# Optimization experiments

Measured on AMD Instinct MI355X. Metric: run time of the kernel, lower is better.

Reference implementation:

```python
import jax, jax.numpy as jnp
import numpy as np

EMBED = 768
HIDDEN = 768
HEADS = 12
HEAD_DIM = HIDDEN // HEADS


def setup_inputs() -> dict:
    key = jax.random.key(0)
    ks = jax.random.split(key, 9)
    B, S = 16, 512
    lim = 1.0 / np.sqrt(EMBED)
    def lin(kw, kb):
        W = jax.random.uniform(kw, (EMBED, HIDDEN), jnp.float32, -lim, lim)
        b = jax.random.uniform(kb, (HIDDEN,), jnp.float32, -lim, lim)
        return W, b
    Wq, bq = lin(ks[0], ks[1])
    Wk, bk = lin(ks[2], ks[3])
    Wv, bv = lin(ks[4], ks[5])
    inp = jax.random.normal(ks[6], (B, S, EMBED), jnp.float32)
    mask = jax.random.randint(ks[7], (B, S), 0, 2).astype(jnp.float32)
    return {"input": inp, "input_mask": mask,
            "Wq": Wq, "bq": bq, "Wk": Wk, "bk": bk, "Wv": Wv, "bv": bv}


def reference(input, input_mask, Wq, bq, Wk, bk, Wv, bv):
    B, S, _ = input.shape
    # projections -> (B, H, S, D)
    def proj(W, b):
        x = jnp.einsum('bse,eh->bsh', input, W) + b
        return x.reshape(B, S, HEADS, HEAD_DIM).transpose(0, 2, 1, 3)
    Q = proj(Wq, bq)
    K = proj(Wk, bk)
    V = proj(Wv, bv)
    # scores (B, H, S, S), additive mask over keys
    scores = jnp.einsum('bhqd,bhkd->bhqk', Q, K) / jnp.sqrt(jnp.float32(HEAD_DIM))
    bias = (input_mask * -1e9)[:, None, None, :]  # (B,1,1,S) broadcast over heads & queries
    weight = jax.nn.softmax(scores + bias, axis=-1)
    out = jnp.einsum('bhqk,bhkd->bhqd', weight, V)
    return out.transpose(0, 2, 1, 3).reshape(B, S, HIDDEN)
```

## Files before the change

### kernel.cpp

```cpp
#include <hip/hip_runtime.h>
#include <hip/hip_bf16.h>
#include <cstdint>
#include <cstddef>

#define B_  16
#define S_  512
#define E_  768
#define NH_ 12
#define D_  64
#define M_  (B_*S_)

typedef unsigned short u16;
typedef __attribute__((ext_vector_type(4))) float f32x4;
typedef __attribute__((ext_vector_type(8))) short bf16x8;

#define LOG2E 1.4426950408889634f

__device__ __forceinline__ u16 f2bf(float f){
  union { float fv; uint32_t u; } v; v.fv = f;
  uint32_t u = v.u;
  uint32_t r = u + 0x7fffu + ((u >> 16) & 1u);
  return (u16)(r >> 16);
}

__device__ __forceinline__ void gload_lds16(const u16* g, u16* l){
  __builtin_amdgcn_global_load_lds(
      (const __attribute__((address_space(1))) void*)g,
      (__attribute__((address_space(3))) void*)l, 16, 0, 0);
}

__device__ __forceinline__ uint4 pack8(const float4& a, const float4& b){
  float2 p01; p01.x = a.x; p01.y = a.y;
  float2 p23; p23.x = a.z; p23.y = a.w;
  float2 p45; p45.x = b.x; p45.y = b.y;
  float2 p67; p67.x = b.z; p67.y = b.w;
  __hip_bfloat162 h0 = __float22bfloat162_rn(p01);
  __hip_bfloat162 h1 = __float22bfloat162_rn(p23);
  __hip_bfloat162 h2 = __float22bfloat162_rn(p45);
  __hip_bfloat162 h3 = __float22bfloat162_rn(p67);
  uint4 r;
  r.x = *reinterpret_cast<const unsigned int*>(&h0);
  r.y = *reinterpret_cast<const unsigned int*>(&h1);
  r.z = *reinterpret_cast<const unsigned int*>(&h2);
  r.w = *reinterpret_cast<const unsigned int*>(&h3);
  return r;
}

__global__ __launch_bounds__(256) void prep_kernel(
    const float* __restrict__ Wq, const float* __restrict__ Wk,
    const float* __restrict__ Wv, u16* __restrict__ WtBase)
{
  __shared__ float t[32][33];
  const int tt = blockIdx.x;
  int z = tt / 576, rem = tt % 576;
  int byi = rem / 24, bxi = rem % 24;
  const float* W = (z == 0) ? Wq : ((z == 1) ? Wk : Wv);
  u16* Wt = WtBase + (size_t)z * E_ * E_;
  int bx0 = bxi * 32, by0 = byi * 32;
  int tx = threadIdx.x & 31, ty = threadIdx.x >> 5;
  #pragma unroll
  for (int i = 0; i < 32; i += 8)
    t[ty + i][tx] = W[(size_t)(by0 + ty + i) * E_ + bx0 + tx];
  __syncthreads();
  #pragma unroll
  for (int i = 0; i < 32; i += 8)
    Wt[(size_t)(bx0 + ty + i) * E_ + by0 + tx] = f2bf(t[tx][ty + i]);
}

__global__ __launch_bounds__(512) void qkv_gemm_kernel(
    const float* __restrict__ X, const u16* __restrict__ WtBase,
    const float* __restrict__ bq, const float* __restrict__ bk, const float* __restrict__ bv,
    u16* __restrict__ Qb, u16* __restrict__ Kb, u16* __restrict__ VtB)
{
  extern __shared__ u16 lds[];
  u16* ldsA = lds;
  u16* ldsB = lds + 2 * 8192;

  const int z = blockIdx.z;
  const u16* Wt = WtBase + (size_t)z * E_ * E_;
  const float* bias = (z == 0) ? bq : ((z == 1) ? bk : bv);
  const int m0 = blockIdx.x * 128;
  const int n0 = blockIdx.y * 256;
  const int tid = threadIdx.x;
  const int lane = tid & 63;
  const int wave = tid >> 6;
  const int wm = wave & 1, wn = wave >> 1;
  const int col0 = lane & 15, quad = lane >> 4;
  const int rslot = quad*16 + (col0 ^ (quad << 1));
  const int oct_l = lane >> 4;
  const int row_l = (lane & 15) ^ (oct_l << 1);

  f32x4 acc[4][4];
  #pragma unroll
  for (int i = 0; i < 4; ++i)
    #pragma unroll
    for (int j = 0; j < 4; ++j)
      acc[i][j] = (f32x4){0.f, 0.f, 0.f, 0.f};

  const float* pX  = X  + (size_t)(m0 + wave*16 + row_l) * E_ + oct_l*8;
  const u16*   pB0 = Wt + (size_t)(n0 + wave*32 + row_l) * E_ + oct_l*8;
  const u16*   pB1 = pB0 + (size_t)16 * E_;

  float4 ax[4];
  auto loadA = [&](int k0){
    const float* p0 = pX + k0;
    const float* p1 = pX + k0 + 32;
    ax[0] = *reinterpret_cast<const float4*>(p0);
    ax[1] = *reinterpret_cast<const float4*>(p0 + 4);
    ax[2] = *reinterpret_cast<const float4*>(p1);
    ax[3] = *reinterpret_cast<const float4*>(p1 + 4);
  };
  auto writeA = [&](int buf){
    u16* la = ldsA + buf * 8192;
    uint4 w0 = pack8(ax[0], ax[1]);
    uint4 w1 = pack8(ax[2], ax[3]);
    *reinterpret_cast<uint4*>(&la[(2*wave    )*512 + lane*8]) = w0;
    *reinterpret_cast<uint4*>(&la[(2*wave + 1)*512 + lane*8]) = w1;
  };
  auto stageB = [&](int k0, int buf){
    u16* lb = ldsB + buf * 16384;
    gload_lds16(pB0 + k0,      lb + (4*wave    )*512);
    gload_lds16(pB0 + k0 + 32, lb + (4*wave + 1)*512);
    gload_lds16(pB1 + k0,      lb + (4*wave + 2)*512);
    gload_lds16(pB1 + k0 + 32, lb + (4*wave + 3)*512);
  };

  auto compute = [&](int buf){
    const u16* la = ldsA + buf * 8192;
    const u16* lb = ldsB + buf * 16384;
    #pragma unroll
    for (int ks = 0; ks < 2; ++ks){
      bf16x8 af[4], bfr[4];
      #pragma unroll
      for (int mi = 0; mi < 4; ++mi)
        af[mi] = *reinterpret_cast<const bf16x8*>(&la[((wm*4 + mi)*2 + ks)*512 + rslot*8]);
      #pragma unroll
      for (int ni = 0; ni < 4; ++ni)
        bfr[ni] = *reinterpret_cast<const bf16x8*>(&lb[((wn*4 + ni)*2 + ks)*512 + rslot*8]);
      #pragma unroll
      for (int mi = 0; mi < 4; ++mi)
        #pragma unroll
        for (int ni = 0; ni < 4; ++ni)
          acc[mi][ni] = __builtin_amdgcn_mfma_f32_16x16x32_bf16(af[mi], bfr[ni], acc[mi][ni], 0, 0, 0);
    }
  };

  stageB(0, 0);
  loadA(0);
  writeA(0);

  #pragma unroll 1
  for (int st = 0; st < 12; ++st){
    const int cur = st & 1;
    __syncthreads();
    if (st < 11){
      stageB((st + 1) * 64, cur ^ 1);
      loadA((st + 1) * 64);
    }
    compute(cur);
    if (st < 11) writeA(cur ^ 1);
  }

  #pragma unroll
  for (int mi = 0; mi < 4; ++mi){
    #pragma unroll
    for (int ni = 0; ni < 4; ++ni){
      int n = n0 + wn*64 + ni*16 + col0;
      float bval = bias[n];
      int h = n >> 6, d = n & 63;
      #pragma unroll
      for (int r = 0; r < 4; ++r){
        int m = m0 + wm*64 + mi*16 + quad*4 + r;
        int b = m >> 9, s = m & 511;
        u16 obf = f2bf(acc[mi][ni][r] + bval);
        size_t bh = (size_t)b * NH_ + h;
        if (z == 0)      Qb[(bh * S_ + s) * D_ + d] = obf;
        else if (z == 1) Kb[(bh * S_ + s) * D_ + d] = obf;
        else             VtB[(bh * D_ + d) * S_ + s] = obf;
      }
    }
  }
}

__global__ __launch_bounds__(256) void attn_kernel(
    const u16* __restrict__ Qb, const u16* __restrict__ Kb, const u16* __restrict__ VtB,
    const float* __restrict__ mask, float* __restrict__ out)
{
  __shared__ u16 lK[2][8 * 512];
  __shared__ u16 lV[2][8 * 512];
  __shared__ u16 lP[8 * 1024];
  __shared__ float biasS[S_];
  const int bh = blockIdx.x;
  const int qt = blockIdx.y;
  const int b = bh / NH_, h = bh % NH_;
  const int tid = threadIdx.x, lane = tid & 63, wave = tid >> 6;
  const int col0 = lane & 15, quad = lane >> 4;
  const int ls = lane & 15, lk = lane >> 4;
  const float C1 = 0.125f * LOG2E;

  for (int i = tid; i < S_; i += 256)
    biasS[i] = mask[b * S_ + i] * (-1.0e9f * LOG2E);

  const u16* Kbh = Kb  + (size_t)bh * S_ * D_;
  const u16* Vbh = VtB + (size_t)bh * D_ * S_;

  bf16x8 qf[2][2];
  #pragma unroll
  for (int g = 0; g < 2; ++g){
    int qrow = qt*128 + wave*32 + g*16 + col0;
    #pragma unroll
    for (int ks = 0; ks < 2; ++ks)
      qf[g][ks] = *reinterpret_cast<const bf16x8*>(
          Qb + ((size_t)bh * S_ + qrow) * D_ + ks*32 + quad*8);
  }

  uint4 rg[4];
  auto issue = [&](int st){
    if (wave < 2){
      #pragma unroll
      for (int gg = 0; gg < 4; ++gg){
        int c = wave*4 + gg, ks = c >> 2, nt = c & 3;
        rg[gg] = *reinterpret_cast<const uint4*>(
            Kbh + (size_t)(st*64 + nt*16 + ls) * D_ + ks*32 + lk*8);
      }
    } else {
      #pragma unroll
      for (int gg = 0; gg < 4; ++gg){
        int c = (wave - 2)*4 + gg, ks2 = c >> 2, nd = c & 3;
        rg[gg] = *reinterpret_cast<const uint4*>(
            Vbh + (size_t)(nd*16 + ls) * S_ + st*64 + ks2*32 + lk*8);
      }
    }
  };
  issue(0);

  f32x4 o[2][4];
  #pragma unroll
  for (int g = 0; g < 2; ++g)
    #pragma unroll
    for (int i = 0; i < 4; ++i) o[g][i] = (f32x4){0.f, 0.f, 0.f, 0.f};
  float psum[2] = {0.f, 0.f};

  #pragma unroll 1
  for (int st = 0; st < 8; ++st){
    const int cur = st & 1;
    if (wave < 2){
      #pragma unroll
      for (int gg = 0; gg < 4; ++gg)
        *reinterpret_cast<uint4*>(&lK[cur][(wave*4 + gg)*512 + lane*8]) = rg[gg];
    } else {
      #pragma unroll
      for (int gg = 0; gg < 4; ++gg)
        *reinterpret_cast<uint4*>(&lV[cur][((wave - 2)*4 + gg)*512 + lane*8]) = rg[gg];
    }
    __syncthreads();
    if (st < 7) issue(st + 1);

    f32x4 sc[2][4];
    #pragma unroll
    for (int g = 0; g < 2; ++g)
      #pragma unroll
      for (int nt = 0; nt < 4; ++nt) sc[g][nt] = (f32x4){0.f, 0.f, 0.f, 0.f};
    #pragma unroll
    for (int ks = 0; ks < 2; ++ks){
      bf16x8 kf[4];
      #pragma unroll
      for (int nt = 0; nt < 4; ++nt)
        kf[nt] = *reinterpret_cast<const bf16x8*>(&lK[cur][(ks*4 + nt)*512 + lane*8]);
      #pragma unroll
      for (int g = 0; g < 2; ++g)
        #pragma unroll
        for (int nt = 0; nt < 4; ++nt)
          sc[g][nt] = __builtin_amdgcn_mfma_f32_16x16x32_bf16(kf[nt], qf[g][ks], sc[g][nt], 0, 0, 0);
    }

    float4 bb[4];
    #pragma unroll
    for (int nt = 0; nt < 4; ++nt)
      bb[nt] = *reinterpret_cast<const float4*>(&biasS[st*64 + nt*16 + quad*4]);

    #pragma unroll
    for (int g = 0; g < 2; ++g){
      #pragma unroll
      for (int nt = 0; nt < 4; ++nt){
        float p0 = exp2f(sc[g][nt][0] * C1 + bb[nt].x);
        float p1 = exp2f(sc[g][nt][1] * C1 + bb[nt].y);
        float p2 = exp2f(sc[g][nt][2] * C1 + bb[nt].z);
        float p3 = exp2f(sc[g][nt][3] * C1 + bb[nt].w);
        psum[g] += (p0 + p1) + (p2 + p3);
        float2 ab; ab.x = p0; ab.y = p1;
        float2 cd; cd.x = p2; cd.y = p3;
        __hip_bfloat162 h01 = __float22bfloat162_rn(ab);
        __hip_bfloat162 h23 = __float22bfloat162_rn(cd);
        uint2 pw;
        pw.x = *reinterpret_cast<unsigned int*>(&h01);
        pw.y = *reinterpret_cast<unsigned int*>(&h23);
        int addr = (wave*2 + g)*1024 + (nt >> 1)*512
                 + (((nt & 1)*2 + (quad >> 1))*16 + col0)*8 + (quad & 1)*4;
        *reinterpret_cast<uint2*>(&lP[addr]) = pw;
      }
    }

    #pragma unroll
    for (int ks2 = 0; ks2 < 2; ++ks2){
      bf16x8 pf0 = *reinterpret_cast<const bf16x8*>(&lP[(wave*2 + 0)*1024 + ks2*512 + lane*8]);
      bf16x8 pf1 = *reinterpret_cast<const bf16x8*>(&lP[(wave*2 + 1)*1024 + ks2*512 + lane*8]);
      #pragma unroll
      for (int nd = 0; nd < 4; ++nd){
        bf16x8 vf = *reinterpret_cast<const bf16x8*>(&lV[cur][(ks2*4 + nd)*512 + lane*8]);
        o[0][nd] = __builtin_amdgcn_mfma_f32_16x16x32_bf16(pf0, vf, o[0][nd], 0, 0, 0);
        o[1][nd] = __builtin_amdgcn_mfma_f32_16x16x32_bf16(pf1, vf, o[1][nd], 0, 0, 0);
      }
    }
  }

  #pragma unroll
  for (int g = 0; g < 2; ++g){
    float tot = psum[g];
    tot += __shfl_xor(tot, 16, 64);
    tot += __shfl_xor(tot, 32, 64);
    #pragma unroll
    for (int r = 0; r < 4; ++r){
      int s = qt*128 + wave*32 + g*16 + quad*4 + r;
      float lr = __shfl(tot, (lane & 48) | (quad*4 + r), 64);
      float inv = 1.0f / lr;
      #pragma unroll
      for (int nd = 0; nd < 4; ++nd){
        int d = nd*16 + col0;
        out[((size_t)b * S_ + s) * E_ + h*D_ + d] = o[g][nd][r] * inv;
      }
    }
  }
}

extern "C" void kernel_launch(void* const* d_in, const int* in_sizes, int n_in,
                              void* d_out, int out_size, void* d_ws, size_t ws_size,
                              hipStream_t stream){
  const float* X    = (const float*)d_in[0];
  const float* mask = (const float*)d_in[1];
  const float* Wq   = (const float*)d_in[2];
  const float* bq   = (const float*)d_in[3];
  const float* Wk   = (const float*)d_in[4];
  const float* bk   = (const float*)d_in[5];
  const float* Wv   = (const float*)d_in[6];
  const float* bv   = (const float*)d_in[7];
  float* out = (float*)d_out;

  u16* Wt = (u16*)d_ws;
  u16* Qb = Wt + (size_t)3 * E_ * E_;
  u16* Kb = Qb + (size_t)M_ * E_;
  u16* Vt = Kb + (size_t)M_ * E_;

  prep_kernel<<<1728, 256, 0, stream>>>(Wq, Wk, Wv, Wt);
  qkv_gemm_kernel<<<dim3(64, 3, 3), 512, 98304, stream>>>(X, Wt, bq, bk, bv, Qb, Kb, Vt);
  attn_kernel<<<dim3(192, 4), 256, 0, stream>>>(Qb, Kb, Vt, mask, out);
}
```

Baseline: 228.3 us.

## Fuse QKV projection and attention into one per-(batch,head) kernel

Replaces the separate QKV GEMM and attention kernels with one kernel per (batch, head). Each block computes Q, K and V for all 512 tokens of its head directly into LDS, then runs attention from LDS, so Q/K/V never go through global memory. Block indices are mapped so that related blocks share an XCD. The costs are that only 192 blocks of 512 threads run, each with about 146KB of LDS (low occupancy). X is also read directly from global without LDS staging, and each block rereads its batch's X rows once for each of Q, K and V.

```diff
diff --git a/kernel.cpp b/kernel.cpp
--- a/kernel.cpp
+++ b/kernel.cpp
@@ -67,226 +67,170 @@
     Wt[(size_t)(bx0 + ty + i) * E_ + by0 + tx] = f2bf(t[tx][ty + i]);
 }
 
-__global__ __launch_bounds__(512) void qkv_gemm_kernel(
+__global__ __launch_bounds__(512) void fused_kernel(
     const float* __restrict__ X, const u16* __restrict__ WtBase,
     const float* __restrict__ bq, const float* __restrict__ bk, const float* __restrict__ bv,
-    u16* __restrict__ Qb, u16* __restrict__ Kb, u16* __restrict__ VtB)
+    const float* __restrict__ mask, float* __restrict__ out)
 {
   extern __shared__ u16 lds[];
-  u16* ldsA = lds;
-  u16* ldsB = lds + 2 * 8192;
-
-  const int z = blockIdx.z;
-  const u16* Wt = WtBase + (size_t)z * E_ * E_;
-  const float* bias = (z == 0) ? bq : ((z == 1) ? bk : bv);
-  const int m0 = blockIdx.x * 128;
-  const int n0 = blockIdx.y * 256;
-  const int tid = threadIdx.x;
-  const int lane = tid & 63;
-  const int wave = tid >> 6;
-  const int wm = wave & 1, wn = wave >> 1;
+  u16* lK  = lds;
+  u16* lV  = lds + 32768;
+  u16* lBP = lds + 65536;
+  float* biasS = (float*)(lds + 73728);
+
+  const int blk = blockIdx.x;
+  const int xcd = blk & 7, idx = blk >> 3;
+  const int b = xcd * 2 + (idx >= 12 ? 1 : 0);
+  const int h = (idx >= 12) ? (idx - 12) : idx;
+
+  const int tid = threadIdx.x, lane = tid & 63, wave = tid >> 6;
   const int col0 = lane & 15, quad = lane >> 4;
   const int rslot = quad*16 + (col0 ^ (quad << 1));
   const int oct_l = lane >> 4;
   const int row_l = (lane & 15) ^ (oct_l << 1);
+  const float C1 = 0.125f * LOG2E;
+
+  if (tid < S_) biasS[tid] = mask[b * S_ + tid] * (-1.0e9f * LOG2E);
+
+  const float* Xrow = X + ((size_t)(b * S_ + wave * 64)) * E_;
 
   f32x4 acc[4][4];
   #pragma unroll
   for (int i = 0; i < 4; ++i)
     #pragma unroll
-    for (int j = 0; j < 4; ++j)
-      acc[i][j] = (f32x4){0.f, 0.f, 0.f, 0.f};
-
-  const float* pX  = X  + (size_t)(m0 + wave*16 + row_l) * E_ + oct_l*8;
-  const u16*   pB0 = Wt + (size_t)(n0 + wave*32 + row_l) * E_ + oct_l*8;
-  const u16*   pB1 = pB0 + (size_t)16 * E_;
-
-  float4 ax[4];
-  auto loadA = [&](int k0){
-    const float* p0 = pX + k0;
-    const float* p1 = pX + k0 + 32;
-    ax[0] = *reinterpret_cast<const float4*>(p0);
-    ax[1] = *reinterpret_cast<const float4*>(p0 + 4);
-    ax[2] = *reinterpret_cast<const float4*>(p1);
-    ax[3] = *reinterpret_cast<const float4*>(p1 + 4);
+    for (int j = 0; j < 4; ++j) acc[i][j] = (f32x4){0.f,0.f,0.f,0.f};
+
+  bf16x8 qf[4][2];
+
+  auto stageB = [&](int t, int buf){
+    int zt = t / 12, kt = t % 12;
+    const u16* src = WtBase + (size_t)zt * E_ * E_
+                   + (size_t)(h*64 + (wave>>1)*16 + row_l) * E_
+                   + kt*64 + (wave & 1)*32 + oct_l*8;
+    gload_lds16(src, lBP + buf*4096 + wave*512);
   };
-  auto writeA = [&](int buf){
-    u16* la = ldsA + buf * 8192;
-    uint4 w0 = pack8(ax[0], ax[1]);
-    uint4 w1 = pack8(ax[2], ax[3]);
-    *reinterpret_cast<uint4*>(&la[(2*wave    )*512 + lane*8]) = w0;
-    *reinterpret_cast<uint4*>(&la[(2*wave + 1)*512 + lane*8]) = w1;
-  };
-  auto stageB = [&](int k0, int buf){
-    u16* lb = ldsB + buf * 16384;
-    gload_lds16(pB0 + k0,      lb + (4*wave    )*512);
-    gload_lds16(pB0 + k0 + 32, lb + (4*wave + 1)*512);
-    gload_lds16(pB1 + k0,      lb + (4*wave + 2)*512);
-    gload_lds16(pB1 + k0 + 32, lb + (4*wave + 3)*512);
-  };
-
-  auto compute = [&](int buf){
-    const u16* la = ldsA + buf * 8192;
-    const u16* lb = ldsB + buf * 16384;
+
+  stageB(0, 0);
+
+  #pragma unroll 1
+  for (int t = 0; t < 36; ++t){
+    __syncthreads();
+    if (t < 35) stageB(t + 1, (t + 1) & 1);
+    const int kt = t % 12;
+    const u16* lb = lBP + (t & 1) * 4096;
     #pragma unroll
     for (int ks = 0; ks < 2; ++ks){
-      bf16x8 af[4], bfr[4];
-      #pragma unroll
-      for (int mi = 0; mi < 4; ++mi)
-        af[mi] = *reinterpret_cast<const bf16x8*>(&la[((wm*4 + mi)*2 + ks)*512 + rslot*8]);
+      bf16x8 bfr[4], af[4];
       #pragma unroll
       for (int ni = 0; ni < 4; ++ni)
-        bfr[ni] = *reinterpret_cast<const bf16x8*>(&lb[((wn*4 + ni)*2 + ks)*512 + rslot*8]);
+        bfr[ni] = *reinterpret_cast<const bf16x8*>(&lb[(ni*2 + ks)*512 + rslot*8]);
+      #pragma unroll
+      for (int mi = 0; mi < 4; ++mi){
+        const float* p = Xrow + (size_t)(mi*16 + col0) * E_ + kt*64 + ks*32 + quad*8;
+        float4 a0 = *reinterpret_cast<const float4*>(p);
+        float4 a1 = *reinterpret_cast<const float4*>(p + 4);
+        uint4 u = pack8(a0, a1);
+        af[mi] = *reinterpret_cast<const bf16x8*>(&u);
+      }
       #pragma unroll
       for (int mi = 0; mi < 4; ++mi)
         #pragma unroll
         for (int ni = 0; ni < 4; ++ni)
           acc[mi][ni] = __builtin_amdgcn_mfma_f32_16x16x32_bf16(af[mi], bfr[ni], acc[mi][ni], 0, 0, 0);
     }
-  };
-
-  stageB(0, 0);
-  loadA(0);
-  writeA(0);
-
-  #pragma unroll 1
-  for (int st = 0; st < 12; ++st){
-    const int cur = st & 1;
-    __syncthreads();
-    if (st < 11){
-      stageB((st + 1) * 64, cur ^ 1);
-      loadA((st + 1) * 64);
-    }
-    compute(cur);
-    if (st < 11) writeA(cur ^ 1);
+    if (kt == 11){
+      const int z = t / 12;
+      const float* bz = (z == 0) ? bq : ((z == 1) ? bk : bv);
+      float bvv[4];
+      #pragma unroll
+      for (int ni = 0; ni < 4; ++ni) bvv[ni] = bz[h*64 + ni*16 + col0];
+      if (z < 2){
+        u16* dst = (z == 0) ? lV : lK;
+        #pragma unroll
+        for (int mi = 0; mi < 4; ++mi)
+          #pragma unroll
+          for (int ni = 0; ni < 4; ++ni){
+            int chunk = (z == 0) ? (wave*8 + mi*2 + (ni>>1))
+                                 : (wave*8 + (ni>>1)*4 + mi);
+            int base = chunk*512 + (((ni&1)*2 + (col0>>3))*16 + quad*4)*8 + (col0 & 7);
+            #pragma unroll
+            for (int r = 0; r < 4; ++r)
+              dst[base + r*8] = f2bf(acc[mi][ni][r] + bvv[ni]);
+          }
+        if (z == 0){
+          #pragma unroll
+          for (int g = 0; g < 4; ++g)
+            #pragma unroll
+            for (int ks = 0; ks < 2; ++ks)
+              qf[g][ks] = *reinterpret_cast<const bf16x8*>(&lV[(wave*8 + g*2 + ks)*512 + lane*8]);
+        }
+      } else {
+        #pragma unroll
+        for (int mi = 0; mi < 4; ++mi)
+          #pragma unroll
+          for (int ni = 0; ni < 4; ++ni){
+            int chunk = wave*8 + ((mi & 2) >> 1)*4 + ni;
+            int off = chunk*512 + (((mi&1)*2 + (quad>>1))*16 + col0)*8 + (quad & 1)*4;
+            float2 ab; ab.x = acc[mi][ni][0] + bvv[ni]; ab.y = acc[mi][ni][1] + bvv[ni];
+            float2 cd; cd.x = acc[mi][ni][2] + bvv[ni]; cd.y = acc[mi][ni][3] + bvv[ni];
+            __hip_bfloat162 h01 = __float22bfloat162_rn(ab);
+            __hip_bfloat162 h23 = __float22bfloat162_rn(cd);
+            uint2 pw;
+            pw.x = *reinterpret_cast<unsigned int*>(&h01);
+            pw.y = *reinterpret_cast<unsigned int*>(&h23);
+            *reinterpret_cast<uint2*>(&lV[off]) = pw;
+          }
+      }
+      #pragma unroll
+      for (int i = 0; i < 4; ++i)
+        #pragma unroll
+        for (int j = 0; j < 4; ++j) acc[i][j] = (f32x4){0.f,0.f,0.f,0.f};
+    }
   }
-
-  #pragma unroll
-  for (int mi = 0; mi < 4; ++mi){
-    #pragma unroll
-    for (int ni = 0; ni < 4; ++ni){
-      int n = n0 + wn*64 + ni*16 + col0;
-      float bval = bias[n];
-      int h = n >> 6, d = n & 63;
-      #pragma unroll
-      for (int r = 0; r < 4; ++r){
-        int m = m0 + wm*64 + mi*16 + quad*4 + r;
-        int b = m >> 9, s = m & 511;
-        u16 obf = f2bf(acc[mi][ni][r] + bval);
-        size_t bh = (size_t)b * NH_ + h;
-        if (z == 0)      Qb[(bh * S_ + s) * D_ + d] = obf;
-        else if (z == 1) Kb[(bh * S_ + s) * D_ + d] = obf;
-        else             VtB[(bh * D_ + d) * S_ + s] = obf;
-      }
-    }
-  }
-}
-
-__global__ __launch_bounds__(256) void attn_kernel(
-    const u16* __restrict__ Qb, const u16* __restrict__ Kb, const u16* __restrict__ VtB,
-    const float* __restrict__ mask, float* __restrict__ out)
-{
-  __shared__ u16 lK[2][8 * 512];
-  __shared__ u16 lV[2][8 * 512];
-  __shared__ u16 lP[8 * 1024];
-  __shared__ float biasS[S_];
-  const int bh = blockIdx.x;
-  const int qt = blockIdx.y;
-  const int b = bh / NH_, h = bh % NH_;
-  const int tid = threadIdx.x, lane = tid & 63, wave = tid >> 6;
-  const int col0 = lane & 15, quad = lane >> 4;
-  const int ls = lane & 15, lk = lane >> 4;
-  const float C1 = 0.125f * LOG2E;
-
-  for (int i = tid; i < S_; i += 256)
-    biasS[i] = mask[b * S_ + i] * (-1.0e9f * LOG2E);
-
-  const u16* Kbh = Kb  + (size_t)bh * S_ * D_;
-  const u16* Vbh = VtB + (size_t)bh * D_ * S_;
-
-  bf16x8 qf[2][2];
-  #pragma unroll
-  for (int g = 0; g < 2; ++g){
-    int qrow = qt*128 + wave*32 + g*16 + col0;
-    #pragma unroll
-    for (int ks = 0; ks < 2; ++ks)
-      qf[g][ks] = *reinterpret_cast<const bf16x8*>(
-          Qb + ((size_t)bh * S_ + qrow) * D_ + ks*32 + quad*8);
-  }
-
-  uint4 rg[4];
-  auto issue = [&](int st){
-    if (wave < 2){
-      #pragma unroll
-      for (int gg = 0; gg < 4; ++gg){
-        int c = wave*4 + gg, ks = c >> 2, nt = c & 3;
-        rg[gg] = *reinterpret_cast<const uint4*>(
-            Kbh + (size_t)(st*64 + nt*16 + ls) * D_ + ks*32 + lk*8);
-      }
-    } else {
-      #pragma unroll
-      for (int gg = 0; gg < 4; ++gg){
-        int c = (wave - 2)*4 + gg, ks2 = c >> 2, nd = c & 3;
-        rg[gg] = *reinterpret_cast<const uint4*>(
-            Vbh + (size_t)(nd*16 + ls) * S_ + st*64 + ks2*32 + lk*8);
-      }
-    }
-  };
-  issue(0);
-
-  f32x4 o[2][4];
-  #pragma unroll
-  for (int g = 0; g < 2; ++g)
-    #pragma unroll
-    for (int i = 0; i < 4; ++i) o[g][i] = (f32x4){0.f, 0.f, 0.f, 0.f};
-  float psum[2] = {0.f, 0.f};
+  __syncthreads();
+
+  f32x4 o[4][4];
+  #pragma unroll
+  for (int g = 0; g < 4; ++g)
+    #pragma unroll
+    for (int i = 0; i < 4; ++i) o[g][i] = (f32x4){0.f,0.f,0.f,0.f};
+  float psum[4] = {0.f, 0.f, 0.f, 0.f};
+  u16* lP = lBP + wave * 1024;
 
   #pragma unroll 1
   for (int st = 0; st < 8; ++st){
-    const int cur = st & 1;
-    if (wave < 2){
-      #pragma unroll
-      for (int gg = 0; gg < 4; ++gg)
-        *reinterpret_cast<uint4*>(&lK[cur][(wave*4 + gg)*512 + lane*8]) = rg[gg];
-    } else {
-      #pragma unroll
-      for (int gg = 0; gg < 4; ++gg)
-        *reinterpret_cast<uint4*>(&lV[cur][((wave - 2)*4 + gg)*512 + lane*8]) = rg[gg];
-    }
-    __syncthreads();
-    if (st < 7) issue(st + 1);
-
-    f32x4 sc[2][4];
-    #pragma unroll
-    for (int g = 0; g < 2; ++g)
-      #pragma unroll
-      for (int nt = 0; nt < 4; ++nt) sc[g][nt] = (f32x4){0.f, 0.f, 0.f, 0.f};
-    #pragma unroll
-    for (int ks = 0; ks < 2; ++ks){
-      bf16x8 kf[4];
+    bf16x8 kf[2][4], vf[2][4];
+    #pragma unroll
+    for (int ks = 0; ks < 2; ++ks)
       #pragma unroll
       for (int nt = 0; nt < 4; ++nt)
-        kf[nt] = *reinterpret_cast<const bf16x8*>(&lK[cur][(ks*4 + nt)*512 + lane*8]);
-      #pragma unroll
-      for (int g = 0; g < 2; ++g)
-        #pragma unroll
-        for (int nt = 0; nt < 4; ++nt)
-          sc[g][nt] = __builtin_amdgcn_mfma_f32_16x16x32_bf16(kf[nt], qf[g][ks], sc[g][nt], 0, 0, 0);
-    }
-
+        kf[ks][nt] = *reinterpret_cast<const bf16x8*>(&lK[(st*8 + ks*4 + nt)*512 + lane*8]);
+    #pragma unroll
+    for (int ks2 = 0; ks2 < 2; ++ks2)
+      #pragma unroll
+      for (int nd = 0; nd < 4; ++nd)
+        vf[ks2][nd] = *reinterpret_cast<const bf16x8*>(&lV[(st*8 + ks2*4 + nd)*512 + lane*8]);
     float4 bb[4];
     #pragma unroll
     for (int nt = 0; nt < 4; ++nt)
       bb[nt] = *reinterpret_cast<const float4*>(&biasS[st*64 + nt*16 + quad*4]);
 
     #pragma unroll
-    for (int g = 0; g < 2; ++g){
+    for (int g = 0; g < 4; ++g){
+      f32x4 sc[4];
+      #pragma unroll
+      for (int nt = 0; nt < 4; ++nt) sc[nt] = (f32x4){0.f,0.f,0.f,0.f};
+      #pragma unroll
+      for (int ks = 0; ks < 2; ++ks)
+        #pragma unroll
+        for (int nt = 0; nt < 4; ++nt)
+          sc[nt] = __builtin_amdgcn_mfma_f32_16x16x32_bf16(kf[ks][nt], qf[g][ks], sc[nt], 0, 0, 0);
       #pragma unroll
       for (int nt = 0; nt < 4; ++nt){
-        float p0 = exp2f(sc[g][nt][0] * C1 + bb[nt].x);
-        float p1 = exp2f(sc[g][nt][1] * C1 + bb[nt].y);
-        float p2 = exp2f(sc[g][nt][2] * C1 + bb[nt].z);
-        float p3 = exp2f(sc[g][nt][3] * C1 + bb[nt].w);
+        float p0 = exp2f(sc[nt][0] * C1 + bb[nt].x);
+        float p1 = exp2f(sc[nt][1] * C1 + bb[nt].y);
+        float p2 = exp2f(sc[nt][2] * C1 + bb[nt].z);
+        float p3 = exp2f(sc[nt][3] * C1 + bb[nt].w);
         psum[g] += (p0 + p1) + (p2 + p3);
         float2 ab; ab.x = p0; ab.y = p1;
         float2 cd; cd.x = p2; cd.y = p3;
@@ -295,33 +239,27 @@
         uint2 pw;
         pw.x = *reinterpret_cast<unsigned int*>(&h01);
         pw.y = *reinterpret_cast<unsigned int*>(&h23);
-        int addr = (wave*2 + g)*1024 + (nt >> 1)*512
-                 + (((nt & 1)*2 + (quad >> 1))*16 + col0)*8 + (quad & 1)*4;
+        int addr = (nt >> 1)*512 + (((nt & 1)*2 + (quad >> 1))*16 + col0)*8 + (quad & 1)*4;
         *reinterpret_cast<uint2*>(&lP[addr]) = pw;
       }
-    }
-
-    #pragma unroll
-    for (int ks2 = 0; ks2 < 2; ++ks2){
-      bf16x8 pf0 = *reinterpret_cast<const bf16x8*>(&lP[(wave*2 + 0)*1024 + ks2*512 + lane*8]);
-      bf16x8 pf1 = *reinterpret_cast<const bf16x8*>(&lP[(wave*2 + 1)*1024 + ks2*512 + lane*8]);
-      #pragma unroll
-      for (int nd = 0; nd < 4; ++nd){
-        bf16x8 vf = *reinterpret_cast<const bf16x8*>(&lV[cur][(ks2*4 + nd)*512 + lane*8]);
-        o[0][nd] = __builtin_amdgcn_mfma_f32_16x16x32_bf16(pf0, vf, o[0][nd], 0, 0, 0);
-        o[1][nd] = __builtin_amdgcn_mfma_f32_16x16x32_bf16(pf1, vf, o[1][nd], 0, 0, 0);
+      #pragma unroll
+      for (int ks2 = 0; ks2 < 2; ++ks2){
+        bf16x8 pf = *reinterpret_cast<const bf16x8*>(&lP[ks2*512 + lane*8]);
+        #pragma unroll
+        for (int nd = 0; nd < 4; ++nd)
+          o[g][nd] = __builtin_amdgcn_mfma_f32_16x16x32_bf16(pf, vf[ks2][nd], o[g][nd], 0, 0, 0);
       }
     }
   }
 
   #pragma unroll
-  for (int g = 0; g < 2; ++g){
+  for (int g = 0; g < 4; ++g){
     float tot = psum[g];
     tot += __shfl_xor(tot, 16, 64);
     tot += __shfl_xor(tot, 32, 64);
     #pragma unroll
     for (int r = 0; r < 4; ++r){
-      int s = qt*128 + wave*32 + g*16 + quad*4 + r;
+      int s = wave*64 + g*16 + quad*4 + r;
       float lr = __shfl(tot, (lane & 48) | (quad*4 + r), 64);
       float inv = 1.0f / lr;
       #pragma unroll
@@ -347,11 +285,7 @@
   float* out = (float*)d_out;
 
   u16* Wt = (u16*)d_ws;
-  u16* Qb = Wt + (size_t)3 * E_ * E_;
-  u16* Kb = Qb + (size_t)M_ * E_;
-  u16* Vt = Kb + (size_t)M_ * E_;
 
   prep_kernel<<<1728, 256, 0, stream>>>(Wq, Wk, Wv, Wt);
-  qkv_gemm_kernel<<<dim3(64, 3, 3), 512, 98304, stream>>>(X, Wt, bq, bk, bv, Qb, Kb, Vt);
-  attn_kernel<<<dim3(192, 4), 256, 0, stream>>>(Qb, Kb, Vt, mask, out);
-}
+  fused_kernel<<<192, 512, 149504, stream>>>(X, Wt, bq, bk, bv, mask, out);
+}
```

After: 274.5 us. 1.2x slower.
